# Kernel optimization log

Hardware: AMD Instinct MI355X
Metric: run time of the kernel (lower is better)

The kernel has to match this reference:

```python
import jax, jax.numpy as jnp
import numpy as np

NUM_HEADS = 8
NUM_Q = 64
RANK = 64
DIM = 768
LN_EPS = 1e-5


def setup_inputs() -> dict:
    key = jax.random.key(0)
    ks = jax.random.split(key, 8)
    b, n = 4, 1024
    x = jax.random.normal(ks[0], (b, NUM_Q, DIM), dtype=jnp.float32)
    context = jax.random.normal(ks[1], (b, n, DIM), dtype=jnp.float32)
    s = 0.02
    Wq = jax.random.normal(ks[2], (DIM, DIM), dtype=jnp.float32) * s
    Wk = jax.random.normal(ks[3], (DIM, DIM), dtype=jnp.float32) * s
    Wv1 = jax.random.normal(ks[4], (DIM, NUM_Q * RANK), dtype=jnp.float32) * s
    ln_g = jnp.ones((NUM_Q * RANK,), dtype=jnp.float32)
    ln_b = jnp.zeros((NUM_Q * RANK,), dtype=jnp.float32)
    Wc = jax.random.normal(ks[5], (NUM_Q, RANK, DIM), dtype=jnp.float32) * s
    Wout = jax.random.normal(ks[6], (DIM, DIM), dtype=jnp.float32) * s
    return {"x": x, "context": context, "Wq": Wq, "Wk": Wk, "Wv1": Wv1,
            "ln_g": ln_g, "ln_b": ln_b, "Wc": Wc, "Wout": Wout}


def reference(x, context, Wq, Wk, Wv1, ln_g, ln_b, Wc, Wout):
    b, nq, d = x.shape
    n = context.shape[1]
    h, dh = NUM_HEADS, d // NUM_HEADS

    q = x @ Wq                      # [b, nq, d]
    k = context @ Wk                # [b, n, d]

    # q-aware V: Linear -> LayerNorm(all_q_mid) -> grouped 1x1 conv (per-query rank->d)
    h1 = context @ Wv1              # [b, n, NUM_Q*RANK]
    mu = jnp.mean(h1, axis=-1, keepdims=True)
    var = jnp.var(h1, axis=-1, keepdims=True)
    h1 = (h1 - mu) * jax.lax.rsqrt(var + LN_EPS) * ln_g + ln_b
    vmid = h1.reshape(b, n, NUM_Q, RANK)
    v = jnp.einsum('bnqr,qrd->bqnd', vmid, Wc)   # [b, NUM_Q, n, d]
    # split heads: 'b q n (h dh) -> b h q n dh'
    v = v.reshape(b, NUM_Q, n, h, dh).transpose(0, 3, 1, 2, 4)

    qh = q.reshape(b, nq, h, dh).transpose(0, 2, 1, 3)   # [b,h,nq,dh]
    kh = k.reshape(b, n, h, dh).transpose(0, 2, 1, 3)    # [b,h,n,dh]
    scale = dh ** (-0.25)
    sim = jnp.einsum('bhid,bhjd->bhij', qh * scale, kh * scale)
    attn = jax.nn.softmax(sim, axis=-1)                  # [b,h,nq,n]
    out = jnp.einsum('bhij,bhijd->bhid', attn, v)        # per-query V
    out = out.transpose(0, 2, 1, 3).reshape(b, nq, d)
    return out @ Wout
```

## Files before the change

kernel.cpp:

```cpp
#include <hip/hip_runtime.h>
#include <math.h>

typedef unsigned short ushort_t;
typedef __bf16 bf16x8 __attribute__((ext_vector_type(8)));
typedef float f32x4 __attribute__((ext_vector_type(4)));

__device__ __forceinline__ ushort_t f2b_rne(float f) {
    union { float f; unsigned int u; } c;
    c.f = f;
    unsigned int u = c.u;
    u += 0x7FFFu + ((u >> 16) & 1u);
    return (ushort_t)(u >> 16);
}
__device__ __forceinline__ float b2f(ushort_t v) {
    union { unsigned int u; float f; } c;
    c.u = ((unsigned int)v) << 16;
    return c.f;
}

__device__ __forceinline__ void gl_lds16(const ushort_t* g, ushort_t* l) {
    __builtin_amdgcn_global_load_lds(
        (const __attribute__((address_space(1))) void*)g,
        (__attribute__((address_space(3))) void*)l, 16, 0, 0);
}

__global__ __launch_bounds__(256) void prep(
    const float* __restrict__ x, const float* __restrict__ context,
    const float* __restrict__ Wq, const float* __restrict__ Wk,
    const float* __restrict__ Wv1, const float* __restrict__ Wout,
    ushort_t* __restrict__ x_b, ushort_t* __restrict__ ctx_b,
    ushort_t* __restrict__ Wq_t, ushort_t* __restrict__ Wk_t,
    ushort_t* __restrict__ Wv1_t, ushort_t* __restrict__ Wout_b,
    float* __restrict__ colzero,
    int b, int n) {
    const int t = threadIdx.x;
    const int bid = blockIdx.x;
    const int nb_x = (b * 64 * 768 / 4) / 256;
    const int nb_c = (b * n * 768 / 4) / 256;

    if (bid < nb_x + nb_c) {
        const float* in = (bid < nb_x) ? x : context;
        ushort_t* outp = (bid < nb_x) ? x_b : ctx_b;
        const int i = ((bid < nb_x) ? bid : (bid - nb_x)) * 256 + t;
        float4 v = ((const float4*)in)[i];
        ushort_t o[4] = {f2b_rne(v.x), f2b_rne(v.y), f2b_rne(v.z), f2b_rne(v.w)};
        *(uint2*)&outp[(size_t)i * 4] = *(uint2*)o;
        return;
    }

    int u = bid - nb_x - nb_c;
    if (u >= 4800) {
        const int idx = (u - 4800) * 256 + t;
        ((float4*)colzero)[idx] = make_float4(0.f, 0.f, 0.f, 0.f);
        return;
    }
    if (u >= 4224) {
        const int i = (u - 4224) * 256 + t;
        float4 v = ((const float4*)Wout)[i];
        ushort_t o[4] = {f2b_rne(v.x), f2b_rne(v.y), f2b_rne(v.z), f2b_rne(v.w)};
        *(uint2*)&Wout_b[(size_t)i * 4] = *(uint2*)o;
        return;
    }

    const float* in;
    ushort_t* outp;
    int R = 768, C = 768;
    if (u < 576)        { in = Wq;  outp = Wq_t; }
    else if (u < 1152)  { u -= 576;  in = Wk;  outp = Wk_t; }
    else                { u -= 1152; in = Wv1; outp = Wv1_t; C = 4096; }
    const int ct = C / 32;
    const int c0 = (u % ct) * 32, r0 = (u / ct) * 32;
    const int tx = t & 31, ty = t >> 5;

    __shared__ float tt[32][33];
#pragma unroll
    for (int i = 0; i < 4; i++)
        tt[ty + 8 * i][tx] = in[(size_t)(r0 + ty + 8 * i) * C + c0 + tx];
    __syncthreads();
#pragma unroll
    for (int i = 0; i < 4; i++)
        outp[(size_t)(c0 + ty + 8 * i) * R + r0 + tx] = f2b_rne(tt[tx][ty + 8 * i]);
}

__device__ __forceinline__ void gemm_tile_big(
    const ushort_t* __restrict__ A, const ushort_t* __restrict__ Bt,
    ushort_t* __restrict__ C, int N, int row0, int col0, ushort_t* lds) {
    constexpr int K = 768;
    constexpr int NSTEP = 24;
    constexpr int SLOT = 512 * 32;

    const int t = threadIdx.x;
    const int lane = t & 63, wave = t >> 6;
    const int quad = lane >> 4, l15 = lane & 15;
    const int wm = (wave >> 2) * 128;
    const int wn = (wave & 3) * 64;

    const int srow = lane >> 2;
    const int sslot = (lane & 3) ^ ((lane >> 3) & 3);
    const ushort_t* gA = A + (size_t)(row0 + wave * 32 + srow) * K + sslot * 8;
    const ushort_t* gB = Bt + (size_t)(col0 + wave * 32 + srow) * K + sslot * 8;
    const int ldsA = wave * 1024;
    const int ldsB = 256 * 32 + wave * 1024;

    const int rslot = (quad ^ ((l15 >> 1) & 3)) * 8;
    const int abase = (wm + l15) * 32 + rslot;
    const int bbase = 256 * 32 + (wn + l15) * 32 + rslot;

    f32x4 acc[8][4] = {};
    bf16x8 af[8], bfr[4];

    auto STAGE_A = [&](int s) {
        const int rg = (s & 3) * SLOT;
        const int ko = s * 32;
        gl_lds16(gA + ko, lds + rg + ldsA);
        gl_lds16(gA + 16 * K + ko, lds + rg + ldsA + 512);
    };
    auto STAGE_B = [&](int s) {
        const int rg = (s & 3) * SLOT;
        const int ko = s * 32;
        gl_lds16(gB + ko, lds + rg + ldsB);
        gl_lds16(gB + 16 * K + ko, lds + rg + ldsB + 512);
    };
    auto READ_B = [&](int s) {
        const ushort_t* p = lds + (s & 3) * SLOT + bbase;
#pragma unroll
        for (int j = 0; j < 4; ++j) bfr[j] = *(const bf16x8*)&p[j * 512];
    };
    auto READ_A_LO = [&](int s) {
        const ushort_t* p = lds + (s & 3) * SLOT + abase;
#pragma unroll
        for (int i = 0; i < 4; ++i) af[i] = *(const bf16x8*)&p[i * 512];
    };
    auto READ_A_HI = [&](int s) {
        const ushort_t* p = lds + (s & 3) * SLOT + abase;
#pragma unroll
        for (int i = 4; i < 8; ++i) af[i] = *(const bf16x8*)&p[i * 512];
    };
    auto MFMA_LO = [&]() {
        __builtin_amdgcn_s_setprio(1);
#pragma unroll
        for (int i = 0; i < 4; ++i)
#pragma unroll
            for (int j = 0; j < 4; ++j)
                acc[i][j] = __builtin_amdgcn_mfma_f32_16x16x32_bf16(
                    af[i], bfr[j], acc[i][j], 0, 0, 0);
        __builtin_amdgcn_s_setprio(0);
    };
    auto MFMA_HI = [&]() {
        __builtin_amdgcn_s_setprio(1);
#pragma unroll
        for (int i = 4; i < 8; ++i)
#pragma unroll
            for (int j = 0; j < 4; ++j)
                acc[i][j] = __builtin_amdgcn_mfma_f32_16x16x32_bf16(
                    af[i], bfr[j], acc[i][j], 0, 0, 0);
        __builtin_amdgcn_s_setprio(0);
    };

    STAGE_A(0); STAGE_B(0);
    STAGE_A(1); STAGE_B(1);
    STAGE_A(2); STAGE_B(2);
    asm volatile("s_waitcnt vmcnt(8)" ::: "memory");
    __builtin_amdgcn_s_barrier();

    for (int s = 0; s < NSTEP - 3; ++s) {
        READ_B(s);
        READ_A_LO(s);
        STAGE_A(s + 3);
        __builtin_amdgcn_sched_barrier(0);
        __builtin_amdgcn_s_barrier();
        asm volatile("s_waitcnt lgkmcnt(0)" ::: "memory");
        __builtin_amdgcn_sched_barrier(0);
        MFMA_LO();
        __builtin_amdgcn_sched_barrier(0);
        __builtin_amdgcn_s_barrier();
        READ_A_HI(s);
        STAGE_B(s + 3);
        asm volatile("s_waitcnt vmcnt(8)" ::: "memory");
        __builtin_amdgcn_sched_barrier(0);
        __builtin_amdgcn_s_barrier();
        asm volatile("s_waitcnt lgkmcnt(0)" ::: "memory");
        __builtin_amdgcn_sched_barrier(0);
        MFMA_HI();
        __builtin_amdgcn_sched_barrier(0);
        __builtin_amdgcn_s_barrier();
    }

    asm volatile("s_waitcnt vmcnt(0)" ::: "memory");
    __builtin_amdgcn_s_barrier();
#pragma unroll
    for (int s = NSTEP - 3; s < NSTEP; ++s) {
        READ_B(s);
        READ_A_LO(s);
        READ_A_HI(s);
        asm volatile("s_waitcnt lgkmcnt(0)" ::: "memory");
        __builtin_amdgcn_sched_barrier(0);
        MFMA_LO();
        MFMA_HI();
    }

#pragma unroll
    for (int i = 0; i < 8; ++i)
#pragma unroll
        for (int j = 0; j < 4; ++j)
#pragma unroll
            for (int r = 0; r < 4; ++r) {
                const int row = row0 + wm + i * 16 + quad * 4 + r;
                const int col = col0 + wn + j * 16 + l15;
                C[(size_t)row * N + col] = f2b_rne(acc[i][j][r]);
            }
}

__device__ __forceinline__ void gemm_tile_small(
    const ushort_t* __restrict__ A, const ushort_t* __restrict__ Bt,
    ushort_t* __restrict__ C, int N, int row0, int col0, ushort_t* lds) {
    constexpr int K = 768;
    constexpr int NSTEP = 24;
    constexpr int SLOT = 256 * 32;

    const int t = threadIdx.x;
    const int lane = t & 63, wave = t >> 6;
    const int quad = lane >> 4, l15 = lane & 15;
    const int wm = (wave >> 2) * 64;
    const int wn = (wave & 3) * 32;

    const int srow = lane >> 2;
    const int sslot = (lane & 3) ^ ((lane >> 3) & 3);
    const ushort_t* gA = A + (size_t)(row0 + wave * 16 + srow) * K + sslot * 8;
    const ushort_t* gB = Bt + (size_t)(col0 + wave * 16 + srow) * K + sslot * 8;
    const int ldsA = wave * 512;
    const int ldsB = 128 * 32 + wave * 512;

    const int rslot = (quad ^ ((l15 >> 1) & 3)) * 8;
    const int abase = (wm + l15) * 32 + rslot;
    const int bbase = 128 * 32 + (wn + l15) * 32 + rslot;

    f32x4 acc[4][2] = {};

    auto STAGE = [&](int s) {
        const int rg = (s & 3) * SLOT;
        const int ko = s * 32;
        gl_lds16(gA + ko, lds + rg + ldsA);
        gl_lds16(gB + ko, lds + rg + ldsB);
    };

    auto COMPUTE = [&](int s) {
        const int rg = (s & 3) * SLOT;
        const ushort_t* pA = lds + rg + abase;
        const ushort_t* pB = lds + rg + bbase;
        bf16x8 af[4], bfr[2];
#pragma unroll
        for (int i = 0; i < 4; ++i) af[i] = *(const bf16x8*)&pA[i * 512];
#pragma unroll
        for (int j = 0; j < 2; ++j) bfr[j] = *(const bf16x8*)&pB[j * 512];
        __builtin_amdgcn_s_setprio(1);
#pragma unroll
        for (int i = 0; i < 4; ++i)
#pragma unroll
            for (int j = 0; j < 2; ++j)
                acc[i][j] = __builtin_amdgcn_mfma_f32_16x16x32_bf16(
                    af[i], bfr[j], acc[i][j], 0, 0, 0);
        __builtin_amdgcn_s_setprio(0);
    };

    STAGE(0); STAGE(1); STAGE(2);

    for (int s = 0; s < NSTEP - 3; ++s) {
        __builtin_amdgcn_sched_barrier(0);
        __builtin_amdgcn_s_barrier();
        STAGE(s + 3);
        asm volatile("s_waitcnt vmcnt(6)" ::: "memory");
        __builtin_amdgcn_s_barrier();
        __builtin_amdgcn_sched_barrier(0);
        COMPUTE(s);
    }
    __builtin_amdgcn_sched_barrier(0);
    __builtin_amdgcn_s_barrier();
    asm volatile("s_waitcnt vmcnt(0)" ::: "memory");
    __builtin_amdgcn_s_barrier();
    __builtin_amdgcn_sched_barrier(0);
    COMPUTE(NSTEP - 3);
    COMPUTE(NSTEP - 2);
    COMPUTE(NSTEP - 1);

#pragma unroll
    for (int i = 0; i < 4; ++i)
#pragma unroll
        for (int j = 0; j < 2; ++j)
#pragma unroll
            for (int r = 0; r < 4; ++r) {
                const int row = row0 + wm + i * 16 + quad * 4 + r;
                const int col = col0 + wn + j * 16 + l15;
                C[(size_t)row * N + col] = f2b_rne(acc[i][j][r]);
            }
}

__global__ __launch_bounds__(512, 2) void gemm_ring(
    const ushort_t* __restrict__ x_b, const ushort_t* __restrict__ ctx_b,
    const ushort_t* __restrict__ Wq_t, const ushort_t* __restrict__ Wk_t,
    const ushort_t* __restrict__ Wv1_t,
    ushort_t* __restrict__ qb, ushort_t* __restrict__ kb,
    ushort_t* __restrict__ h1t, int b, int n) {
    extern __shared__ ushort_t lds[];
    const int Mn = b * n;
    const int M = b * 64;
    const int nbig = 16 * (Mn / 256);
    const int nk = (Mn / 128) * 6;
    int u = blockIdx.x;
    if (u < nbig) {
        gemm_tile_big(Wv1_t, ctx_b, h1t, Mn, (u & 15) * 256, (u >> 4) * 256,
                      lds);
    } else if ((u -= nbig) < nk) {
        const int rt = Mn / 128;
        gemm_tile_small(ctx_b, Wk_t, kb, 768, (u % rt) * 128, (u / rt) * 128,
                        lds);
    } else {
        u -= nk;
        const int rt = M / 128;
        gemm_tile_small(x_b, Wq_t, qb, 768, (u % rt) * 128, (u / rt) * 128,
                        lds);
    }
}

__global__ __launch_bounds__(256) void scores_stats(
    const ushort_t* __restrict__ qb, const ushort_t* __restrict__ kb,
    const ushort_t* __restrict__ h1t, float* __restrict__ S,
    float* __restrict__ colsum, float* __restrict__ colsumsq,
    int b, int n, int Mn) {
    __shared__ ushort_t sb[192 * 104];
    const int t = threadIdx.x;
    const int nsc = b * 8 * (n / 128);

    if (blockIdx.x >= nsc) {
        const int u = blockIdx.x - nsc;
        const int rc = u >> 4;
        const int cc = u & 15;
        const int cg = t & 31;
        const int rg = t >> 5;
        const ushort_t* p =
            h1t + (size_t)(rc * 256 + rg * 32) * Mn + cc * 256 + cg * 8;
        float s[8] = {}, s2[8] = {};
#pragma unroll 4
        for (int r = 0; r < 32; r++) {
            const bf16x8 v = *(const bf16x8*)&p[(size_t)r * Mn];
#pragma unroll
            for (int j = 0; j < 8; j++) {
                const float f = (float)v[j];
                s[j] += f;
                s2[j] += f * f;
            }
        }
        float* red = (float*)sb;
#pragma unroll
        for (int j = 0; j < 8; j++) {
            red[rg * 256 + cg * 8 + j] = s[j];
            red[2048 + rg * 256 + cg * 8 + j] = s2[j];
        }
        __syncthreads();
        float ts = 0.f, ts2 = 0.f;
#pragma unroll
        for (int g = 0; g < 8; g++) {
            ts += red[g * 256 + t];
            ts2 += red[2048 + g * 256 + t];
        }
        atomicAdd(&colsum[cc * 256 + t], ts);
        atomicAdd(&colsumsq[cc * 256 + t], ts2);
        return;
    }

    const int nt = n / 128;
    const int n0 = (blockIdx.x % nt) * 128;
    const int bh = blockIdx.x / nt;
    const int bb = bh >> 3, h = bh & 7;
    const int lane = t & 63, wave = t >> 6;
    const int quad = lane >> 4, l15 = lane & 15;
    const int wm = (wave >> 1) * 32;
    const int wn = (wave & 1) * 64;

    ushort_t* Qs = sb;
    ushort_t* Ks = sb + 64 * 104;

    for (int g = t; g < 768; g += 256) {
        const int r = g / 12, s = g - r * 12;
        *(bf16x8*)&Qs[r * 104 + s * 8] =
            *(const bf16x8*)&qb[(size_t)(bb * 64 + r) * 768 + h * 96 + s * 8];
    }
    for (int g = t; g < 1536; g += 256) {
        const int r = g / 12, s = g - r * 12;
        *(bf16x8*)&Ks[r * 104 + s * 8] =
            *(const bf16x8*)&kb[(size_t)(bb * n + n0 + r) * 768 + h * 96 + s * 8];
    }
    __syncthreads();

    f32x4 acc[2][4] = {};
#pragma unroll
    for (int ks = 0; ks < 3; ks++) {
        bf16x8 af[2], bfr[4];
#pragma unroll
        for (int i = 0; i < 2; i++)
            af[i] = *(const bf16x8*)&Qs[(wm + i * 16 + l15) * 104 + ks * 32 + quad * 8];
#pragma unroll
        for (int j = 0; j < 4; j++)
            bfr[j] = *(const bf16x8*)&Ks[(wn + j * 16 + l15) * 104 + ks * 32 + quad * 8];
#pragma unroll
        for (int i = 0; i < 2; i++)
#pragma unroll
            for (int j = 0; j < 4; j++)
                acc[i][j] = __builtin_amdgcn_mfma_f32_16x16x32_bf16(
                    af[i], bfr[j], acc[i][j], 0, 0, 0);
    }

    const float sc = 0.10206207261596575f;
    float* Sp = S + (size_t)bh * 64 * n;
#pragma unroll
    for (int i = 0; i < 2; i++)
#pragma unroll
        for (int j = 0; j < 4; j++)
#pragma unroll
            for (int r = 0; r < 4; r++) {
                const int row = wm + i * 16 + quad * 4 + r;
                const int col = n0 + wn + j * 16 + l15;
                Sp[(size_t)row * n + col] = acc[i][j][r] * sc;
            }
}

__global__ __launch_bounds__(1024) void attn_fused(
    const float* __restrict__ S, const float* __restrict__ colsum,
    const float* __restrict__ colsumsq, const ushort_t* __restrict__ h1t,
    const float* __restrict__ ln_g, const float* __restrict__ ln_b,
    const float* __restrict__ Wc, const ushort_t* __restrict__ Wout_b,
    float* __restrict__ out, int n, int Mn) {
    const int bq = blockIdx.x;
    const int bb = bq >> 6, qi = bq & 63;
    const int tid = threadIdx.x;
    const int lane = tid & 63, wv = tid >> 6;
    const int quad = lane >> 4, l15 = lane & 15;

    __shared__ ushort_t sW[9 * 1032];
    __shared__ ushort_t sH[64 * 264];
    __shared__ float sl[8], swmu[8];
    __shared__ float pm[16], pl[16], pwm[16];
    __shared__ float sA[512];
    __shared__ float sO[768];

    float* sMu = (float*)sH;
    float* sRs = (float*)sH + 1024;

    for (int i = tid; i < n; i += 1024) {
        const float cs = colsum[bb * n + i];
        const float cq = colsumsq[bb * n + i];
        const float m = cs * (1.0f / 4096.0f);
        sMu[i] = m;
        sRs[i] = rsqrtf(cq * (1.0f / 4096.0f) - m * m + 1e-5f);
    }
    for (int i = tid; i < 1032; i += 1024) sW[8 * 1032 + i] = 0;
    __syncthreads();

    const int h = wv >> 1;
    const int half = wv & 1;
    const int nh = n >> 1;
    const int i0 = half * nh;
    const float* Sp = S + ((size_t)(bb * 8 + h) * 64 + qi) * n;
    {
        float m = -1e30f;
        for (int i = i0 + lane; i < i0 + nh; i += 64) m = fmaxf(m, Sp[i]);
#pragma unroll
        for (int off = 32; off > 0; off >>= 1) m = fmaxf(m, __shfl_down(m, off));
        if (lane == 0) pm[wv] = m;
    }
    __syncthreads();
    const float mh = fmaxf(pm[2 * h], pm[2 * h + 1]);
    {
        float l = 0.f, wm = 0.f;
        for (int i = i0 + lane; i < i0 + nh; i += 64) {
            const float e = expf(Sp[i] - mh);
            const float w = e * sRs[i];
            const ushort_t wb = f2b_rne(w);
            sW[h * 1032 + i] = wb;
            l += e;
            wm += b2f(wb) * sMu[i];
        }
#pragma unroll
        for (int off = 32; off > 0; off >>= 1) {
            l += __shfl_down(l, off);
            wm += __shfl_down(wm, off);
        }
        if (lane == 0) { pl[wv] = l; pwm[wv] = wm; }
    }
    __syncthreads();
    if (tid < 8) {
        sl[tid] = pl[2 * tid] + pl[2 * tid + 1];
        swmu[tid] = pwm[2 * tid] + pwm[2 * tid + 1];
    }

    const int mrow = (l15 < 8 ? l15 : 8) * 1032;
    f32x4 acc = {};
    const int nch = n >> 8;
    for (int ch = 0; ch < nch; ch++) {
        __syncthreads();
        for (int g = tid; g < 2048; g += 1024) {
            const int row = g >> 5, seg = g & 31;
            *(bf16x8*)&sH[row * 264 + seg * 8] =
                *(const bf16x8*)&h1t[(size_t)(qi * 64 + row) * Mn + bb * n +
                                     ch * 256 + seg * 8];
        }
        __syncthreads();
        if (wv < 4) {
#pragma unroll
            for (int ks = 0; ks < 8; ks++) {
                const bf16x8 af = *(const bf16x8*)&sW[mrow + ch * 256 + ks * 32 + quad * 8];
                const bf16x8 bf = *(const bf16x8*)&sH[(wv * 16 + l15) * 264 + ks * 32 + quad * 8];
                acc = __builtin_amdgcn_mfma_f32_16x16x32_bf16(af, bf, acc, 0, 0, 0);
            }
        }
    }
    __syncthreads();

    if (wv < 4) {
#pragma unroll
        for (int r = 0; r < 4; r++) {
            const int hh = quad * 4 + r;
            if (hh < 8) {
                const int rr = wv * 16 + l15;
                const int c = qi * 64 + rr;
                sA[hh * 64 + rr] =
                    ln_g[c] * ((acc[r] - swmu[hh]) / sl[hh]) + ln_b[c];
            }
        }
    }
    __syncthreads();

    for (int d = tid; d < 768; d += 1024) {
        const int hh = d / 96;
        const float* wp = Wc + (size_t)qi * 49152 + d;
        float a = 0.f;
#pragma unroll
        for (int r = 0; r < 64; r++) a += sA[hh * 64 + r] * wp[(size_t)r * 768];
        sO[d] = b2f(f2b_rne(a));
    }
    __syncthreads();

    float* rbuf = (float*)sH;
    if (tid < 768) {
        const int r0 = tid / 96;
        const int c0 = (tid % 96) * 8;
        const ushort_t* wp = Wout_b + (size_t)(r0 * 96) * 768 + c0;
        float acc8[8] = {};
#pragma unroll 4
        for (int s = 0; s < 96; s++) {
            const float sv = sO[r0 * 96 + s];
            const bf16x8 w8 = *(const bf16x8*)&wp[(size_t)s * 768];
#pragma unroll
            for (int j = 0; j < 8; j++) acc8[j] += sv * (float)w8[j];
        }
#pragma unroll
        for (int j = 0; j < 8; j++) rbuf[r0 * 768 + c0 + j] = acc8[j];
    }
    __syncthreads();
    if (tid < 768) {
        float s = 0.f;
#pragma unroll
        for (int g = 0; g < 8; g++) s += rbuf[g * 768 + tid];
        out[(size_t)bq * 768 + tid] = s;
    }
}

extern "C" void kernel_launch(void* const* d_in, const int* in_sizes, int n_in,
                              void* d_out, int out_size, void* d_ws, size_t ws_size,
                              hipStream_t stream) {
    const float* x       = (const float*)d_in[0];
    const float* context = (const float*)d_in[1];
    const float* Wq      = (const float*)d_in[2];
    const float* Wk      = (const float*)d_in[3];
    const float* Wv1     = (const float*)d_in[4];
    const float* ln_g    = (const float*)d_in[5];
    const float* ln_b    = (const float*)d_in[6];
    const float* Wc      = (const float*)d_in[7];
    const float* Wout    = (const float*)d_in[8];
    float* out = (float*)d_out;

    const int b = in_sizes[0] / (64 * 768);
    const int n = in_sizes[1] / (b * 768);
    const int M  = b * 64;
    const int Mn = b * n;

    float* ws = (float*)d_ws;
    size_t off = 0;
    float* S       = ws + off;  off += (size_t)b * 8 * 64 * n;
    float* colsum  = ws + off;  off += (size_t)Mn;
    float* colsumsq= ws + off;  off += (size_t)Mn;

    ushort_t* us = (ushort_t*)(ws + off);
    size_t uo = 0;
    ushort_t* x_b    = us + uo;  uo += (size_t)M * 768;
    ushort_t* ctx_b  = us + uo;  uo += (size_t)Mn * 768;
    ushort_t* qb     = us + uo;  uo += (size_t)M * 768;
    ushort_t* kb     = us + uo;  uo += (size_t)Mn * 768;
    ushort_t* h1t    = us + uo;  uo += (size_t)Mn * 4096;
    ushort_t* Wq_t   = us + uo;  uo += (size_t)768 * 768;
    ushort_t* Wk_t   = us + uo;  uo += (size_t)768 * 768;
    ushort_t* Wv1_t  = us + uo;  uo += (size_t)4096 * 768;
    ushort_t* Wout_b = us + uo;  uo += (size_t)768 * 768;

    const int nb_x = (M * 768 / 4) / 256;
    const int nb_c = (Mn * 768 / 4) / 256;
    prep<<<nb_x + nb_c + 4800 + 8, 256, 0, stream>>>(
        x, context, Wq, Wk, Wv1, Wout, x_b, ctx_b, Wq_t, Wk_t, Wv1_t, Wout_b,
        colsum, b, n);

    const int nbig = 16 * (Mn / 256);
    const int nk = (Mn / 128) * 6;
    const int nq = (M / 128) * 6;
    static bool attr_done = false;
    if (!attr_done) {
        (void)hipFuncSetAttribute(reinterpret_cast<const void*>(&gemm_ring),
                                  hipFuncAttributeMaxDynamicSharedMemorySize,
                                  131072);
        attr_done = true;
    }
    gemm_ring<<<nbig + nk + nq, 512, 131072, stream>>>(
        x_b, ctx_b, Wq_t, Wk_t, Wv1_t, qb, kb, h1t, b, n);

    scores_stats<<<b * 8 * (n / 128) + 256, 256, 0, stream>>>(
        qb, kb, h1t, S, colsum, colsumsq, b, n, Mn);

    attn_fused<<<M, 1024, 0, stream>>>(S, colsum, colsumsq, h1t, ln_g, ln_b,
                                       Wc, Wout_b, out, n, Mn);
}
```

Measured before the change: 167.6 us.

## Shrink GEMM tiles to 256x128 with double-buffered LDS for higher occupancy

Replaces the 256x256 four-stage ring GEMM for the Wv1 projection with a 256x128 tile using a two-slot LDS buffer, and reshapes the 128x128 K/Q tiles to a 2x4 wave layout with double buffering. Dynamic LDS drops from 128 KB to 48 KB per block and the grid for the big GEMM doubles. The aim is more resident blocks per CU and better load balance across CUs. In exchange the pipeline is shallower, there is less data reuse per tile, and the split-phase MFMA scheduling and setprio hints are gone, so global-load latency may be exposed.

```diff
diff --git a/kernel.cpp b/kernel.cpp
--- a/kernel.cpp
+++ b/kernel.cpp
@@ -82,125 +82,74 @@
         outp[(size_t)(c0 + ty + 8 * i) * R + r0 + tx] = f2b_rne(tt[tx][ty + 8 * i]);
 }
 
-__device__ __forceinline__ void gemm_tile_big(
+__device__ __forceinline__ void gemm_tile_256x128(
     const ushort_t* __restrict__ A, const ushort_t* __restrict__ Bt,
     ushort_t* __restrict__ C, int N, int row0, int col0, ushort_t* lds) {
     constexpr int K = 768;
     constexpr int NSTEP = 24;
-    constexpr int SLOT = 512 * 32;
+    constexpr int SLOT = (256 + 128) * 32;
 
     const int t = threadIdx.x;
     const int lane = t & 63, wave = t >> 6;
     const int quad = lane >> 4, l15 = lane & 15;
-    const int wm = (wave >> 2) * 128;
-    const int wn = (wave & 3) * 64;
+    const int wm = (wave >> 1) * 64;
+    const int wn = (wave & 1) * 64;
 
     const int srow = lane >> 2;
     const int sslot = (lane & 3) ^ ((lane >> 3) & 3);
     const ushort_t* gA = A + (size_t)(row0 + wave * 32 + srow) * K + sslot * 8;
-    const ushort_t* gB = Bt + (size_t)(col0 + wave * 32 + srow) * K + sslot * 8;
+    const ushort_t* gB = Bt + (size_t)(col0 + wave * 16 + srow) * K + sslot * 8;
     const int ldsA = wave * 1024;
-    const int ldsB = 256 * 32 + wave * 1024;
+    const int ldsB = 256 * 32 + wave * 512;
 
     const int rslot = (quad ^ ((l15 >> 1) & 3)) * 8;
     const int abase = (wm + l15) * 32 + rslot;
     const int bbase = 256 * 32 + (wn + l15) * 32 + rslot;
 
-    f32x4 acc[8][4] = {};
-    bf16x8 af[8], bfr[4];
-
-    auto STAGE_A = [&](int s) {
-        const int rg = (s & 3) * SLOT;
+    f32x4 acc[4][4] = {};
+
+    auto STAGE = [&](int s) {
+        const int rg = (s & 1) * SLOT;
         const int ko = s * 32;
         gl_lds16(gA + ko, lds + rg + ldsA);
         gl_lds16(gA + 16 * K + ko, lds + rg + ldsA + 512);
+        gl_lds16(gB + ko, lds + rg + ldsB);
     };
-    auto STAGE_B = [&](int s) {
-        const int rg = (s & 3) * SLOT;
-        const int ko = s * 32;
-        gl_lds16(gB + ko, lds + rg + ldsB);
-        gl_lds16(gB + 16 * K + ko, lds + rg + ldsB + 512);
-    };
-    auto READ_B = [&](int s) {
-        const ushort_t* p = lds + (s & 3) * SLOT + bbase;
-#pragma unroll
-        for (int j = 0; j < 4; ++j) bfr[j] = *(const bf16x8*)&p[j * 512];
-    };
-    auto READ_A_LO = [&](int s) {
-        const ushort_t* p = lds + (s & 3) * SLOT + abase;
-#pragma unroll
-        for (int i = 0; i < 4; ++i) af[i] = *(const bf16x8*)&p[i * 512];
-    };
-    auto READ_A_HI = [&](int s) {
-        const ushort_t* p = lds + (s & 3) * SLOT + abase;
-#pragma unroll
-        for (int i = 4; i < 8; ++i) af[i] = *(const bf16x8*)&p[i * 512];
-    };
-    auto MFMA_LO = [&]() {
-        __builtin_amdgcn_s_setprio(1);
+
+    auto COMPUTE = [&](int s) {
+        const int rg = (s & 1) * SLOT;
+        const ushort_t* pA = lds + rg + abase;
+        const ushort_t* pB = lds + rg + bbase;
+        bf16x8 af[4], bfr[4];
+#pragma unroll
+        for (int i = 0; i < 4; ++i) af[i] = *(const bf16x8*)&pA[i * 512];
+#pragma unroll
+        for (int j = 0; j < 4; ++j) bfr[j] = *(const bf16x8*)&pB[j * 512];
 #pragma unroll
         for (int i = 0; i < 4; ++i)
 #pragma unroll
             for (int j = 0; j < 4; ++j)
                 acc[i][j] = __builtin_amdgcn_mfma_f32_16x16x32_bf16(
                     af[i], bfr[j], acc[i][j], 0, 0, 0);
-        __builtin_amdgcn_s_setprio(0);
     };
-    auto MFMA_HI = [&]() {
-        __builtin_amdgcn_s_setprio(1);
-#pragma unroll
-        for (int i = 4; i < 8; ++i)
-#pragma unroll
-            for (int j = 0; j < 4; ++j)
-                acc[i][j] = __builtin_amdgcn_mfma_f32_16x16x32_bf16(
-                    af[i], bfr[j], acc[i][j], 0, 0, 0);
-        __builtin_amdgcn_s_setprio(0);
-    };
-
-    STAGE_A(0); STAGE_B(0);
-    STAGE_A(1); STAGE_B(1);
-    STAGE_A(2); STAGE_B(2);
-    asm volatile("s_waitcnt vmcnt(8)" ::: "memory");
-    __builtin_amdgcn_s_barrier();
-
-    for (int s = 0; s < NSTEP - 3; ++s) {
-        READ_B(s);
-        READ_A_LO(s);
-        STAGE_A(s + 3);
+
+    STAGE(0);
+    for (int s = 0; s < NSTEP; ++s) {
         __builtin_amdgcn_sched_barrier(0);
         __builtin_amdgcn_s_barrier();
-        asm volatile("s_waitcnt lgkmcnt(0)" ::: "memory");
+        if (s < NSTEP - 1) {
+            STAGE(s + 1);
+            asm volatile("s_waitcnt vmcnt(3)" ::: "memory");
+        } else {
+            asm volatile("s_waitcnt vmcnt(0)" ::: "memory");
+        }
+        __builtin_amdgcn_s_barrier();
         __builtin_amdgcn_sched_barrier(0);
-        MFMA_LO();
-        __builtin_amdgcn_sched_barrier(0);
-        __builtin_amdgcn_s_barrier();
-        READ_A_HI(s);
-        STAGE_B(s + 3);
-        asm volatile("s_waitcnt vmcnt(8)" ::: "memory");
-        __builtin_amdgcn_sched_barrier(0);
-        __builtin_amdgcn_s_barrier();
-        asm volatile("s_waitcnt lgkmcnt(0)" ::: "memory");
-        __builtin_amdgcn_sched_barrier(0);
-        MFMA_HI();
-        __builtin_amdgcn_sched_barrier(0);
-        __builtin_amdgcn_s_barrier();
-    }
-
-    asm volatile("s_waitcnt vmcnt(0)" ::: "memory");
-    __builtin_amdgcn_s_barrier();
-#pragma unroll
-    for (int s = NSTEP - 3; s < NSTEP; ++s) {
-        READ_B(s);
-        READ_A_LO(s);
-        READ_A_HI(s);
-        asm volatile("s_waitcnt lgkmcnt(0)" ::: "memory");
-        __builtin_amdgcn_sched_barrier(0);
-        MFMA_LO();
-        MFMA_HI();
-    }
-
-#pragma unroll
-    for (int i = 0; i < 8; ++i)
+        COMPUTE(s);
+    }
+
+#pragma unroll
+    for (int i = 0; i < 4; ++i)
 #pragma unroll
         for (int j = 0; j < 4; ++j)
 #pragma unroll
@@ -211,18 +160,18 @@
             }
 }
 
-__device__ __forceinline__ void gemm_tile_small(
+__device__ __forceinline__ void gemm_tile_128x128(
     const ushort_t* __restrict__ A, const ushort_t* __restrict__ Bt,
     ushort_t* __restrict__ C, int N, int row0, int col0, ushort_t* lds) {
     constexpr int K = 768;
     constexpr int NSTEP = 24;
-    constexpr int SLOT = 256 * 32;
+    constexpr int SLOT = (128 + 128) * 32;
 
     const int t = threadIdx.x;
     const int lane = t & 63, wave = t >> 6;
     const int quad = lane >> 4, l15 = lane & 15;
-    const int wm = (wave >> 2) * 64;
-    const int wn = (wave & 3) * 32;
+    const int wm = (wave >> 1) * 32;
+    const int wn = (wave & 1) * 64;
 
     const int srow = lane >> 2;
     const int sslot = (lane & 3) ^ ((lane >> 3) & 3);
@@ -235,58 +184,51 @@
     const int abase = (wm + l15) * 32 + rslot;
     const int bbase = 128 * 32 + (wn + l15) * 32 + rslot;
 
-    f32x4 acc[4][2] = {};
+    f32x4 acc[2][4] = {};
 
     auto STAGE = [&](int s) {
-        const int rg = (s & 3) * SLOT;
+        const int rg = (s & 1) * SLOT;
         const int ko = s * 32;
         gl_lds16(gA + ko, lds + rg + ldsA);
         gl_lds16(gB + ko, lds + rg + ldsB);
     };
 
     auto COMPUTE = [&](int s) {
-        const int rg = (s & 3) * SLOT;
+        const int rg = (s & 1) * SLOT;
         const ushort_t* pA = lds + rg + abase;
         const ushort_t* pB = lds + rg + bbase;
-        bf16x8 af[4], bfr[2];
-#pragma unroll
-        for (int i = 0; i < 4; ++i) af[i] = *(const bf16x8*)&pA[i * 512];
-#pragma unroll
-        for (int j = 0; j < 2; ++j) bfr[j] = *(const bf16x8*)&pB[j * 512];
-        __builtin_amdgcn_s_setprio(1);
-#pragma unroll
-        for (int i = 0; i < 4; ++i)
-#pragma unroll
-            for (int j = 0; j < 2; ++j)
+        bf16x8 af[2], bfr[4];
+#pragma unroll
+        for (int i = 0; i < 2; ++i) af[i] = *(const bf16x8*)&pA[i * 512];
+#pragma unroll
+        for (int j = 0; j < 4; ++j) bfr[j] = *(const bf16x8*)&pB[j * 512];
+#pragma unroll
+        for (int i = 0; i < 2; ++i)
+#pragma unroll
+            for (int j = 0; j < 4; ++j)
                 acc[i][j] = __builtin_amdgcn_mfma_f32_16x16x32_bf16(
                     af[i], bfr[j], acc[i][j], 0, 0, 0);
-        __builtin_amdgcn_s_setprio(0);
     };
 
-    STAGE(0); STAGE(1); STAGE(2);
-
-    for (int s = 0; s < NSTEP - 3; ++s) {
+    STAGE(0);
+    for (int s = 0; s < NSTEP; ++s) {
         __builtin_amdgcn_sched_barrier(0);
         __builtin_amdgcn_s_barrier();
-        STAGE(s + 3);
-        asm volatile("s_waitcnt vmcnt(6)" ::: "memory");
+        if (s < NSTEP - 1) {
+            STAGE(s + 1);
+            asm volatile("s_waitcnt vmcnt(2)" ::: "memory");
+        } else {
+            asm volatile("s_waitcnt vmcnt(0)" ::: "memory");
+        }
         __builtin_amdgcn_s_barrier();
         __builtin_amdgcn_sched_barrier(0);
         COMPUTE(s);
     }
-    __builtin_amdgcn_sched_barrier(0);
-    __builtin_amdgcn_s_barrier();
-    asm volatile("s_waitcnt vmcnt(0)" ::: "memory");
-    __builtin_amdgcn_s_barrier();
-    __builtin_amdgcn_sched_barrier(0);
-    COMPUTE(NSTEP - 3);
-    COMPUTE(NSTEP - 2);
-    COMPUTE(NSTEP - 1);
-
-#pragma unroll
-    for (int i = 0; i < 4; ++i)
-#pragma unroll
-        for (int j = 0; j < 2; ++j)
+
+#pragma unroll
+    for (int i = 0; i < 2; ++i)
+#pragma unroll
+        for (int j = 0; j < 4; ++j)
 #pragma unroll
             for (int r = 0; r < 4; ++r) {
                 const int row = row0 + wm + i * 16 + quad * 4 + r;
@@ -304,21 +246,21 @@
     extern __shared__ ushort_t lds[];
     const int Mn = b * n;
     const int M = b * 64;
-    const int nbig = 16 * (Mn / 256);
+    const int nbig = 16 * (Mn / 128);
     const int nk = (Mn / 128) * 6;
     int u = blockIdx.x;
     if (u < nbig) {
-        gemm_tile_big(Wv1_t, ctx_b, h1t, Mn, (u & 15) * 256, (u >> 4) * 256,
-                      lds);
+        gemm_tile_256x128(Wv1_t, ctx_b, h1t, Mn, (u & 15) * 256,
+                          (u >> 4) * 128, lds);
     } else if ((u -= nbig) < nk) {
         const int rt = Mn / 128;
-        gemm_tile_small(ctx_b, Wk_t, kb, 768, (u % rt) * 128, (u / rt) * 128,
-                        lds);
+        gemm_tile_128x128(ctx_b, Wk_t, kb, 768, (u % rt) * 128,
+                          (u / rt) * 128, lds);
     } else {
         u -= nk;
         const int rt = M / 128;
-        gemm_tile_small(x_b, Wq_t, qb, 768, (u % rt) * 128, (u / rt) * 128,
-                        lds);
+        gemm_tile_128x128(x_b, Wq_t, qb, 768, (u % rt) * 128,
+                          (u / rt) * 128, lds);
     }
 }
 
@@ -608,17 +550,17 @@
         x, context, Wq, Wk, Wv1, Wout, x_b, ctx_b, Wq_t, Wk_t, Wv1_t, Wout_b,
         colsum, b, n);
 
-    const int nbig = 16 * (Mn / 256);
+    const int nbig = 16 * (Mn / 128);
     const int nk = (Mn / 128) * 6;
     const int nq = (M / 128) * 6;
     static bool attr_done = false;
     if (!attr_done) {
         (void)hipFuncSetAttribute(reinterpret_cast<const void*>(&gemm_ring),
                                   hipFuncAttributeMaxDynamicSharedMemorySize,
-                                  131072);
+                                  49152);
         attr_done = true;
     }
-    gemm_ring<<<nbig + nk + nq, 512, 131072, stream>>>(
+    gemm_ring<<<nbig + nk + nq, 512, 49152, stream>>>(
         x_b, ctx_b, Wq_t, Wk_t, Wv1_t, qb, kb, h1t, b, n);
 
     scores_stats<<<b * 8 * (n / 128) + 256, 256, 0, stream>>>(
```

New measurement: 168.9 us. No clear change (+0.8%).
